# Performance work log

Measured on AMD Instinct MI355X. Metric: run time of the kernel, lower is better.

Reference implementation:

```python
import jax, jax.numpy as jnp
import numpy as np

B, S, D, H, L = 4, 4096, 64, 8, 4
VOCAB, NCLS = 256, 10
MLP = D * H          # mlp_dim = dim * heads = 512
BS = 256             # block size for banded attention
R = 256              # one-sided radius (sliding_window_size = 512)


def sinusoid_pos_emb(s, d):
    pos = np.arange(s)[:, None].astype(np.float32)
    i = np.arange(d // 2)[None, :].astype(np.float32)
    ang = pos / np.power(10000.0, 2.0 * i / d)
    pe = np.zeros((s, d), np.float32)
    pe[:, 0::2] = np.sin(ang)
    pe[:, 1::2] = np.cos(ang)
    return jnp.asarray(pe)


def layernorm(x, s, b):
    m = x.mean(-1, keepdims=True)
    v = ((x - m) ** 2).mean(-1, keepdims=True)
    return (x - m) * jax.lax.rsqrt(v + 1e-6) * s + b


def sliding_window_attn(x, wq, bq, wk, bk, wv, bv, wo, bo):
    Bx, Sx, Dx = x.shape
    Dh = Dx // H
    nb = Sx // BS

    def proj(w, b2):
        return (x @ w + b2).reshape(Bx, Sx, H, Dh).transpose(0, 2, 1, 3)

    q = proj(wq, bq) / jnp.sqrt(jnp.float32(Dh))
    k = proj(wk, bk)
    v = proj(wv, bv)

    def windows(t):  # [B,H,S,Dh] -> [B,H,nb,3*BS,Dh] (prev | self | next blocks)
        tp = jnp.pad(t, ((0, 0), (0, 0), (BS, BS), (0, 0))).reshape(Bx, H, nb + 2, BS, Dh)
        return jnp.concatenate([tp[:, :, :-2], tp[:, :, 1:-1], tp[:, :, 2:]], axis=3)

    kw, vw = windows(k), windows(v)
    qb = q.reshape(Bx, H, nb, BS, Dh)
    scores = jnp.einsum('bhnqd,bhnkd->bhnqk', qb, kw)      # [B,H,nb,BS,3*BS]

    qpos = jnp.arange(BS)[:, None]
    kpos = jnp.arange(3 * BS)[None, :] - BS
    band = jnp.abs(kpos - qpos) <= R                        # [BS,3*BS]
    kglob = jnp.arange(nb)[:, None, None] * BS + kpos[None]  # [nb,1,3*BS]
    valid = (kglob >= 0) & (kglob < Sx)
    mask = band[None] & valid                                # [nb,BS,3*BS]

    scores = jnp.where(mask[None, None], scores, jnp.float32(-1e30))
    probs = jax.nn.softmax(scores, axis=-1)
    out = jnp.einsum('bhnqk,bhnkd->bhnqd', probs, vw)
    out = out.reshape(Bx, H, Sx, Dh).transpose(0, 2, 1, 3).reshape(Bx, Sx, Dx)
    return out @ wo + bo


def setup_inputs() -> dict:
    key = jax.random.key(0)
    ks = jax.random.split(key, 12)
    g = lambda k, shp: jax.random.normal(k, shp, dtype=jnp.float32) * 0.02
    emb = g(ks[0], (VOCAB, D)).at[0].set(0.0)  # padding_idx=0 row is zeros
    return dict(
        x=jax.random.randint(ks[1], (B, S), 0, VOCAB).astype(jnp.int32),
        emb=emb,
        wq=g(ks[2], (L, D, D)), bq=jnp.zeros((L, D)),
        wk=g(ks[3], (L, D, D)), bk=jnp.zeros((L, D)),
        wv=g(ks[4], (L, D, D)), bv=jnp.zeros((L, D)),
        wo=g(ks[5], (L, D, D)), bo=jnp.zeros((L, D)),
        ln1_s=jnp.ones((L, D)), ln1_b=jnp.zeros((L, D)),
        ln2_s=jnp.ones((L, D)), ln2_b=jnp.zeros((L, D)),
        w1=g(ks[6], (L, D, MLP)), b1=jnp.zeros((L, MLP)),
        w2=g(ks[7], (L, MLP, D)), b2=jnp.zeros((L, D)),
        lnf_s=jnp.ones((D,)), lnf_b=jnp.zeros((D,)),
        wcls=g(ks[8], (D, NCLS)), bcls=jnp.zeros((NCLS,)),
    )


def reference(x, emb, wq, bq, wk, bk, wv, bv, wo, bo, ln1_s, ln1_b, ln2_s, ln2_b, w1, b1, w2, b2, lnf_s, lnf_b, wcls, bcls):
    h = emb[x] + sinusoid_pos_emb(S, D)[None]                 # embedding + fixed pos emb
    for l in range(L):
        a = sliding_window_attn(layernorm(h, ln1_s[l], ln1_b[l]),
                                wq[l], bq[l], wk[l], bk[l], wv[l], bv[l], wo[l], bo[l])
        h = h + a
        y = layernorm(h, ln2_s[l], ln2_b[l])
        y = jax.nn.gelu(y @ w1[l] + b1[l]) @ w2[l] + b2[l]
        h = h + y
    h = layernorm(h, lnf_s, lnf_b)
    pooled = h.mean(axis=1)                                   # classifier_pool='MEAN'
    return pooled @ wcls + bcls
```

## Files before the change

### kernel.cpp

```cpp
#include <hip/hip_runtime.h>
#include <hip/hip_bf16.h>

#define DEV __device__ __forceinline__

typedef __attribute__((ext_vector_type(8))) short bf16x8;
typedef __attribute__((ext_vector_type(4))) float f32x4;
typedef __attribute__((ext_vector_type(16))) float f32x16;

DEV short f2bf(float x){ __hip_bfloat16 h = __float2bfloat16(x); return *(short*)&h; }
DEV unsigned pack2bf(float a, float b){
  return (unsigned)(unsigned short)f2bf(a) | ((unsigned)(unsigned short)f2bf(b) << 16);
}
DEV float gelu_fast(float x){
  float z = 0.7978845608028654f*(x + 0.044715f*x*x*x);
  float e = __expf(-2.f*z);
  return x / (1.f + e);
}

#define SB 4096
#define NT 16384
#define DM 64
#define VST 586

__global__ __launch_bounds__(256) void wconv(
    const float* __restrict__ wq, const float* __restrict__ wk,
    const float* __restrict__ wv, const float* __restrict__ wo,
    const float* __restrict__ w1, const float* __restrict__ w2,
    short* __restrict__ wqT, short* __restrict__ wkT,
    short* __restrict__ wvT, short* __restrict__ woT,
    short* __restrict__ w1T, short* __restrict__ w2T)
{
  int t = blockIdx.x, l = blockIdx.y;
  const float* src; short* dst; int K, N, kt, nt;
  if (t < 16) {
    int m = t >> 2, sub = t & 3; kt = sub >> 1; nt = sub & 1; K = 64; N = 64;
    const float* s4[4] = {wq, wk, wv, wo};
    short*       d4[4] = {wqT, wkT, wvT, woT};
    src = s4[m] + l*4096; dst = d4[m] + l*4096;
  } else if (t < 48) {
    kt = (t-16) >> 4; nt = (t-16) & 15; K = 64; N = 512;
    src = w1 + l*32768; dst = w1T + l*32768;
  } else {
    kt = (t-48) >> 1; nt = (t-48) & 1; K = 512; N = 64;
    src = w2 + l*32768; dst = w2T + l*32768;
  }
  __shared__ float lds[32][33];
  int tx = threadIdx.x & 31, ty = threadIdx.x >> 5;
  int k0 = kt*32, n0 = nt*32;
  #pragma unroll
  for (int j=0;j<4;++j) lds[ty+8*j][tx] = src[(size_t)(k0+ty+8*j)*N + n0 + tx];
  __syncthreads();
  #pragma unroll
  for (int j=0;j<4;++j) {
    int nn = ty+8*j;
    dst[(size_t)(n0+nn)*K + k0 + tx] = f2bf(lds[tx][nn]);
  }
}

DEV void make_frags_ln(const float* rowp, float mean, float inv,
    const float* __restrict__ s, const float* __restrict__ b, int kq,
    bf16x8& a0, bf16x8& a1){
  #pragma unroll
  for (int i=0;i<8;++i) a0[i] = f2bf((rowp[kq*8+i]-mean)*inv*s[kq*8+i]+b[kq*8+i]);
  #pragma unroll
  for (int i=0;i<8;++i) a1[i] = f2bf((rowp[32+kq*8+i]-mean)*inv*s[32+kq*8+i]+b[32+kq*8+i]);
}

template<bool EMBED, bool LAST>
__global__ __launch_bounds__(512,2) void layer_kernel(
    const int* __restrict__ x, const float* __restrict__ emb,
    const unsigned short* __restrict__ qin, const unsigned short* __restrict__ kin,
    const unsigned short* __restrict__ vin,
    const short* __restrict__ woT, const float* __restrict__ bo,
    const float* __restrict__ ln2s, const float* __restrict__ ln2b,
    const short* __restrict__ w1T, const float* __restrict__ b1,
    const short* __restrict__ w2T, const float* __restrict__ b2,
    const float* __restrict__ lns, const float* __restrict__ lnb,
    const short* __restrict__ wqT, const short* __restrict__ wkT, const short* __restrict__ wvT,
    const float* __restrict__ bq, const float* __restrict__ bk, const float* __restrict__ bv,
    unsigned short* __restrict__ qo, unsigned short* __restrict__ ko, unsigned short* __restrict__ vo,
    float* __restrict__ h, float* __restrict__ part)
{
  __shared__ uint4 regA4[4608];
  __shared__ uint4 regB4[4688];
  __shared__ float mu[64], iv[64];

  unsigned short* Ks  = (unsigned short*)regA4;
  unsigned short* abL = (unsigned short*)regA4;
  float (*hN)[68]   = (float(*)[68])((char*)regA4 + 9216);
  float (*facc)[68] = (float(*)[68])((char*)regA4 + 26624);
  unsigned short* Vs = (unsigned short*)regB4;
  short (*mid)[520]  = (short(*)[520])regB4;

  const int bid = blockIdx.x;
  const int row_g0 = bid * 64;
  const int tid = threadIdx.x;
  const int w = tid >> 6, lane = tid & 63;
  const int r = lane & 15, kq = lane >> 4;
  const int srow = tid >> 3, sd8 = tid & 7;

  if constexpr (EMBED) {
    int tg = row_g0 + srow;
    int s = tg & (SB-1);
    int tok = x[tg];
    #pragma unroll
    for (int i=0;i<8;++i) {
      int d = sd8*8 + i;
      float fe = (float)(d & ~1) * (1.0f/64.0f);
      float invk = __expf(-9.210340371976184f * fe);
      float ang = (float)s * invk;
      float pe = (d & 1) ? __cosf(ang) : __sinf(ang);
      float val = emb[tok*DM + d] + pe;
      hN[srow][d] = val;
      h[(size_t)tg*DM + d] = val;
    }
  } else {
    const int bbase = row_g0 & ~(SB-1);
    const int kwin0 = row_g0 - 256;

    for (int idx = tid; idx < 4608; idx += 512) {
      int e = idx >> 3, grp = idx & 7;
      int g = kwin0 + e;
      uint4 kv = make_uint4(0,0,0,0), vv = make_uint4(0,0,0,0);
      if ((unsigned)(g - bbase) < (unsigned)SB) {
        kv = *(const uint4*)(kin + (size_t)g*DM + grp*8);
        vv = *(const uint4*)(vin + (size_t)g*DM + grp*8);
      }
      *(uint4*)(Ks + e*64 + ((grp ^ (e & 7)) << 3)) = kv;
      const unsigned short* pv = (const unsigned short*)&vv;
      #pragma unroll
      for (int d = 0; d < 8; ++d) Vs[(grp*8 + d)*VST + e] = pv[d];
    }
    __syncthreads();

    const int qc = lane & 31;
    const int hf = lane >> 5;

    auto attn_job = [&](int qs, f32x16& oacc, float& lacc) {
      const int qglob = row_g0 + qs*32 + qc;
      bf16x8 qfrag = {};
      if (hf == 0) qfrag = *(const bf16x8*)(qin + (size_t)qglob*DM + w*8);
      for (int t = 0; t <= 16; ++t) {
        const int k0l = qs*32 + 32*t;
        const int k0g = kwin0 + k0l;
        if (k0g > bbase + SB-1 || k0g + 31 < bbase) continue;

        bf16x8 kfrag = {};
        if (hf == 0) {
          int e = k0l + qc;
          kfrag = *(const bf16x8*)(Ks + e*64 + ((w ^ (e & 7)) << 3));
        }
        f32x16 s = __builtin_amdgcn_mfma_f32_32x32x16_bf16(kfrag, qfrag, (f32x16){}, 0, 0, 0);

        float pp[16];
        bool needmask = (t == 0) | (t == 16) | (k0g < bbase) | (k0g + 31 > bbase + SB-1);
        if (needmask) {
          #pragma unroll
          for (int rr = 0; rr < 16; ++rr) {
            int klg = k0g + (rr&3) + 8*(rr>>2) + 4*hf;
            bool ok = ((unsigned)(klg - qglob + 256) <= 512u) &&
                      ((unsigned)(klg - bbase) < (unsigned)SB);
            pp[rr] = ok ? __expf(s[rr]) : 0.f;
          }
        } else {
          #pragma unroll
          for (int rr = 0; rr < 16; ++rr) pp[rr] = __expf(s[rr]);
        }
        #pragma unroll
        for (int rr = 0; rr < 16; ++rr) lacc += pp[rr];

        unsigned pk[8];
        #pragma unroll
        for (int j = 0; j < 8; ++j) pk[j] = pack2bf(pp[2*j], pp[2*j+1]);
        unsigned sw[8];
        #pragma unroll
        for (int j = 0; j < 8; ++j) sw[j] = __shfl_xor(pk[j], 32, 64);

        union { unsigned u[4]; bf16x8 v; } pbA;
        pbA.u[0] = hf ? sw[2] : pk[0];
        pbA.u[1] = hf ? sw[3] : pk[1];
        pbA.u[2] = hf ? pk[2] : sw[0];
        pbA.u[3] = hf ? pk[3] : sw[1];
        bf16x8 va1 = {};
        if (qc < 8) va1 = *(const bf16x8*)(Vs + (w*8 + qc)*VST + k0l + 8*hf);
        oacc = __builtin_amdgcn_mfma_f32_32x32x16_bf16(va1, pbA.v, oacc, 0, 0, 0);

        union { unsigned u[4]; bf16x8 v; } pbB;
        pbB.u[0] = hf ? sw[6] : pk[4];
        pbB.u[1] = hf ? sw[7] : pk[5];
        pbB.u[2] = hf ? pk[6] : sw[4];
        pbB.u[3] = hf ? pk[7] : sw[5];
        bf16x8 va2 = {};
        if (qc < 8) va2 = *(const bf16x8*)(Vs + (w*8 + qc)*VST + k0l + 16 + 8*hf);
        oacc = __builtin_amdgcn_mfma_f32_32x32x16_bf16(va2, pbB.v, oacc, 0, 0, 0);
      }
    };

    f32x16 oacc0 = {}; float la0 = 0.f;
    f32x16 oacc1 = {}; float la1 = 0.f;
    attn_job(0, oacc0, la0);
    attn_job(1, oacc1, la1);
    float rcp0 = 1.f / (la0 + __shfl_xor(la0, 32, 64));
    float rcp1 = 1.f / (la1 + __shfl_xor(la1, 32, 64));
    __syncthreads();

    {
      unsigned short ov[4];
      #pragma unroll
      for (int j = 0; j < 4; ++j) ov[j] = (unsigned short)f2bf(oacc0[j] * rcp0);
      *(uint2*)(abL + (qc)*72 + w*8 + 4*hf) = *(uint2*)ov;
      #pragma unroll
      for (int j = 0; j < 4; ++j) ov[j] = (unsigned short)f2bf(oacc1[j] * rcp1);
      *(uint2*)(abL + (32 + qc)*72 + w*8 + 4*hf) = *(uint2*)ov;
    }
    __syncthreads();

    {
      const int rh = w >> 2, ct = w & 3;
      const int col = ct*16 + r;
      const short* wp = woT + (size_t)col*64 + kq*8;
      bf16x8 wb0 = *(const bf16x8*)(wp);
      bf16x8 wb1 = *(const bf16x8*)(wp + 32);
      #pragma unroll
      for (int rf=0; rf<2; ++rf) {
        const short* abp = (const short*)(abL + (rh*32 + rf*16 + r)*72 + kq*8);
        bf16x8 a0 = *(const bf16x8*)abp;
        bf16x8 a1 = *(const bf16x8*)(abp + 32);
        f32x4 acc = (f32x4){0.f,0.f,0.f,0.f};
        acc = __builtin_amdgcn_mfma_f32_16x16x32_bf16(a0, wb0, acc, 0, 0, 0);
        acc = __builtin_amdgcn_mfma_f32_16x16x32_bf16(a1, wb1, acc, 0, 0, 0);
        #pragma unroll
        for (int j=0;j<4;++j) {
          int rl = rh*32 + rf*16 + kq*4 + j;
          hN[rl][col] = acc[j] + bo[col] + h[(size_t)(row_g0+rl)*DM + col];
        }
      }
    }
  }
  __syncthreads();

  {
    const float* p = &hN[srow][sd8*8];
    float v[8];
    float sum = 0.f;
    #pragma unroll
    for (int i=0;i<8;++i){ v[i] = p[i]; sum += v[i]; }
    sum += __shfl_xor(sum, 1, 64); sum += __shfl_xor(sum, 2, 64); sum += __shfl_xor(sum, 4, 64);
    float mean = sum * (1.f/64.f);
    float sq = 0.f;
    #pragma unroll
    for (int i=0;i<8;++i){ float d = v[i]-mean; sq += d*d; }
    sq += __shfl_xor(sq, 1, 64); sq += __shfl_xor(sq, 2, 64); sq += __shfl_xor(sq, 4, 64);
    if (sd8 == 0) { mu[srow] = mean; iv[srow] = rsqrtf(sq*(1.f/64.f) + 1e-6f); }
  }
  __syncthreads();

  if constexpr (!EMBED) {
    {
      bf16x8 a[4][2];
      #pragma unroll
      for (int rf=0; rf<4; ++rf)
        make_frags_ln(&hN[rf*16 + r][0], mu[rf*16 + r], iv[rf*16 + r], ln2s, ln2b, kq, a[rf][0], a[rf][1]);
      const int gc0 = w*64;
      bf16x8 wb[4][2];
      #pragma unroll
      for (int ct=0; ct<4; ++ct) {
        const short* wp = w1T + (size_t)(gc0 + ct*16 + r)*64 + kq*8;
        wb[ct][0] = *(const bf16x8*)(wp);
        wb[ct][1] = *(const bf16x8*)(wp + 32);
      }
      f32x4 acc1[4][4];
      #pragma unroll
      for (int ct=0;ct<4;++ct)
        #pragma unroll
        for (int rf=0;rf<4;++rf) acc1[ct][rf] = (f32x4){0.f,0.f,0.f,0.f};
      #pragma unroll
      for (int ct=0; ct<4; ++ct)
        #pragma unroll
        for (int rf=0; rf<4; ++rf) {
          acc1[ct][rf] = __builtin_amdgcn_mfma_f32_16x16x32_bf16(a[rf][0], wb[ct][0], acc1[ct][rf], 0, 0, 0);
          acc1[ct][rf] = __builtin_amdgcn_mfma_f32_16x16x32_bf16(a[rf][1], wb[ct][1], acc1[ct][rf], 0, 0, 0);
        }
      __syncthreads();
      #pragma unroll
      for (int ct=0; ct<4; ++ct) {
        int gcol = gc0 + ct*16 + r;
        float bb = b1[gcol];
        #pragma unroll
        for (int rf=0; rf<4; ++rf)
          #pragma unroll
          for (int j=0; j<4; ++j)
            mid[rf*16 + kq*4 + j][gcol] = f2bf(gelu_fast(acc1[ct][rf][j] + bb));
      }
    }
    __syncthreads();

    {
      const int kh = w >> 2, ct2 = w & 3;
      const int col2 = ct2*16 + r;
      bf16x8 wf[8];
      #pragma unroll
      for (int ks=0; ks<8; ++ks)
        wf[ks] = *(const bf16x8*)(w2T + (size_t)col2*512 + kh*256 + ks*32 + kq*8);
      f32x4 acc2[4];
      #pragma unroll
      for (int rf=0;rf<4;++rf) acc2[rf] = (f32x4){0.f,0.f,0.f,0.f};
      #pragma unroll
      for (int ks=0; ks<8; ++ks)
        #pragma unroll
        for (int rf=0; rf<4; ++rf) {
          bf16x8 af = *(const bf16x8*)(&mid[rf*16 + r][kh*256 + ks*32 + kq*8]);
          acc2[rf] = __builtin_amdgcn_mfma_f32_16x16x32_bf16(af, wf[ks], acc2[rf], 0, 0, 0);
        }
      if (kh == 0) {
        #pragma unroll
        for (int rf=0; rf<4; ++rf)
          #pragma unroll
          for (int j=0;j<4;++j)
            facc[rf*16 + kq*4 + j][col2] = acc2[rf][j];
      }
      __syncthreads();
      if (kh == 1) {
        float bb = b2[col2];
        #pragma unroll
        for (int rf=0; rf<4; ++rf)
          #pragma unroll
          for (int j=0;j<4;++j) {
            int rl = rf*16 + kq*4 + j;
            float val = acc2[rf][j] + facc[rl][col2] + bb + hN[rl][col2];
            hN[rl][col2] = val;
            h[(size_t)(row_g0+rl)*DM + col2] = val;
          }
      }
    }
    __syncthreads();

    {
      const float* p = &hN[srow][sd8*8];
      float v[8];
      float sum = 0.f;
      #pragma unroll
      for (int i=0;i<8;++i){ v[i] = p[i]; sum += v[i]; }
      sum += __shfl_xor(sum, 1, 64); sum += __shfl_xor(sum, 2, 64); sum += __shfl_xor(sum, 4, 64);
      float mean = sum * (1.f/64.f);
      float sq = 0.f;
      #pragma unroll
      for (int i=0;i<8;++i){ float d = v[i]-mean; sq += d*d; }
      sq += __shfl_xor(sq, 1, 64); sq += __shfl_xor(sq, 2, 64); sq += __shfl_xor(sq, 4, 64);
      if (sd8 == 0) { mu[srow] = mean; iv[srow] = rsqrtf(sq*(1.f/64.f) + 1e-6f); }
    }
    __syncthreads();
  }

  if constexpr (!LAST) {
    const float qscale = 0.35355339059327373f;
    bf16x8 a[4][2];
    #pragma unroll
    for (int rf=0; rf<4; ++rf)
      make_frags_ln(&hN[rf*16 + r][0], mu[rf*16 + r], iv[rf*16 + r], lns, lnb, kq, a[rf][0], a[rf][1]);
    #pragma unroll
    for (int rep=0; rep<2; ++rep) {
      int jj = w + rep*8;
      if (jj < 12) {
        int m = jj >> 2, ct = jj & 3;
        const short* WT = m==0 ? wqT : (m==1 ? wkT : wvT);
        int col = ct*16 + r;
        const short* wp = WT + (size_t)col*64 + kq*8;
        bf16x8 wb0 = *(const bf16x8*)(wp);
        bf16x8 wb1 = *(const bf16x8*)(wp + 32);
        float bias = (m==0 ? bq : (m==1 ? bk : bv))[col];
        float scale = (m==0) ? qscale : 1.f;
        unsigned short* OPT = m==0 ? qo : (m==1 ? ko : vo);
        #pragma unroll
        for (int rf=0; rf<4; ++rf) {
          f32x4 acc = (f32x4){0.f,0.f,0.f,0.f};
          acc = __builtin_amdgcn_mfma_f32_16x16x32_bf16(a[rf][0], wb0, acc, 0, 0, 0);
          acc = __builtin_amdgcn_mfma_f32_16x16x32_bf16(a[rf][1], wb1, acc, 0, 0, 0);
          #pragma unroll
          for (int j=0;j<4;++j) {
            size_t oi = (size_t)(row_g0 + rf*16 + kq*4 + j)*DM + col;
            OPT[oi] = (unsigned short)f2bf((acc[j] + bias)*scale);
          }
        }
      }
    }
  } else {
    float mean = mu[srow], inv = iv[srow];
    #pragma unroll
    for (int i=0;i<8;++i) {
      int d = sd8*8 + i;
      hN[srow][d] = (hN[srow][d]-mean)*inv*lns[d] + lnb[d];
    }
    __syncthreads();
    if (tid < 64) {
      float s = 0.f;
      #pragma unroll 4
      for (int rr=0; rr<64; ++rr) s += hN[rr][tid];
      part[bid*64 + tid] = s;
    }
  }
}

__global__ __launch_bounds__(256) void pool_finalize(const float* __restrict__ part,
    const float* __restrict__ wcls, const float* __restrict__ bcls, float* __restrict__ out)
{
  int tid = threadIdx.x;
  int b = tid >> 6, d = tid & 63;
  float sum = 0.f;
  #pragma unroll 8
  for (int i = 0; i < 64; ++i) sum += part[(b*64 + i)*64 + d];
  __shared__ float pooled[4][64];
  pooled[b][d] = sum * (1.f/4096.f);
  __syncthreads();
  if (tid < 40) {
    int bb = tid / 10, c = tid % 10;
    float acc = bcls[c];
    #pragma unroll
    for (int dd = 0; dd < 64; ++dd) acc = fmaf(pooled[bb][dd], wcls[dd*10 + c], acc);
    out[tid] = acc;
  }
}

extern "C" void kernel_launch(void* const* d_in, const int* in_sizes, int n_in,
                              void* d_out, int out_size, void* d_ws, size_t ws_size,
                              hipStream_t stream)
{
  const int*   x    = (const int*)d_in[0];
  const float* emb  = (const float*)d_in[1];
  const float* wq   = (const float*)d_in[2];
  const float* bq   = (const float*)d_in[3];
  const float* wk   = (const float*)d_in[4];
  const float* bk   = (const float*)d_in[5];
  const float* wv   = (const float*)d_in[6];
  const float* bv   = (const float*)d_in[7];
  const float* wo   = (const float*)d_in[8];
  const float* bo   = (const float*)d_in[9];
  const float* ln1s = (const float*)d_in[10];
  const float* ln1b = (const float*)d_in[11];
  const float* ln2s = (const float*)d_in[12];
  const float* ln2b = (const float*)d_in[13];
  const float* w1   = (const float*)d_in[14];
  const float* b1   = (const float*)d_in[15];
  const float* w2   = (const float*)d_in[16];
  const float* b2   = (const float*)d_in[17];
  const float* lnfs = (const float*)d_in[18];
  const float* lnfb = (const float*)d_in[19];
  const float* wcls = (const float*)d_in[20];
  const float* bcls = (const float*)d_in[21];
  float* out = (float*)d_out;

  char* wsb = (char*)d_ws;
  const size_t MB = 1u << 20;
  float* h  = (float*)(wsb);
  unsigned short* qA = (unsigned short*)(wsb + 4*MB);
  unsigned short* kA = (unsigned short*)(wsb + 6*MB);
  unsigned short* vA = (unsigned short*)(wsb + 8*MB);
  unsigned short* qB = (unsigned short*)(wsb + 10*MB);
  unsigned short* kB = (unsigned short*)(wsb + 12*MB);
  unsigned short* vB = (unsigned short*)(wsb + 14*MB);
  short* wqT = (short*)(wsb + 16*MB);
  short* wkT = (short*)(wsb + 16*MB + 32*1024);
  short* wvT = (short*)(wsb + 16*MB + 64*1024);
  short* woT = (short*)(wsb + 16*MB + 96*1024);
  short* w1T = (short*)(wsb + 16*MB + 128*1024);
  short* w2T = (short*)(wsb + 16*MB + 384*1024);
  float* part = (float*)(wsb + 17*MB);

  wconv<<<dim3(80,4),256,0,stream>>>(wq,wk,wv,wo,w1,w2, wqT,wkT,wvT,woT,w1T,w2T);

  layer_kernel<true,false><<<256,512,0,stream>>>(
      x, emb, nullptr, nullptr, nullptr,
      nullptr, nullptr, nullptr, nullptr,
      nullptr, nullptr, nullptr, nullptr,
      ln1s, ln1b,
      wqT, wkT, wvT, bq, bk, bv,
      qA, kA, vA, h, nullptr);

  for (int l = 0; l < 4; ++l) {
    unsigned short* qi = (l & 1) ? qB : qA;
    unsigned short* ki = (l & 1) ? kB : kA;
    unsigned short* vi = (l & 1) ? vB : vA;
    unsigned short* qu = (l & 1) ? qA : qB;
    unsigned short* ku = (l & 1) ? kA : kB;
    unsigned short* vu = (l & 1) ? vA : vB;
    if (l < 3) {
      layer_kernel<false,false><<<256,512,0,stream>>>(
          nullptr, nullptr, qi, ki, vi,
          woT+4096*l, bo+64*l, ln2s+64*l, ln2b+64*l,
          w1T+32768*l, b1+512*l, w2T+32768*l, b2+64*l,
          ln1s+64*(l+1), ln1b+64*(l+1),
          wqT+4096*(l+1), wkT+4096*(l+1), wvT+4096*(l+1),
          bq+64*(l+1), bk+64*(l+1), bv+64*(l+1),
          qu, ku, vu, h, nullptr);
    } else {
      layer_kernel<false,true><<<256,512,0,stream>>>(
          nullptr, nullptr, qi, ki, vi,
          woT+4096*l, bo+64*l, ln2s+64*l, ln2b+64*l,
          w1T+32768*l, b1+512*l, w2T+32768*l, b2+64*l,
          lnfs, lnfb,
          nullptr, nullptr, nullptr, nullptr, nullptr, nullptr,
          nullptr, nullptr, nullptr, h, part);
    }
  }
  pool_finalize<<<1,256,0,stream>>>(part, wcls, bcls, out);
}
```

Measured before the change: 184.4 us.

## Double workgroup size to 1024 threads and split per-wave work in half

Result: no change. 182.5 us (-1.0%).

```diff
diff --git a/kernel.cpp b/kernel.cpp
--- a/kernel.cpp
+++ b/kernel.cpp
@@ -67,7 +67,7 @@
 }
 
 template<bool EMBED, bool LAST>
-__global__ __launch_bounds__(512,2) void layer_kernel(
+__global__ __launch_bounds__(1024,1) void layer_kernel(
     const int* __restrict__ x, const float* __restrict__ emb,
     const unsigned short* __restrict__ qin, const unsigned short* __restrict__ kin,
     const unsigned short* __restrict__ vin,
@@ -97,15 +97,15 @@
   const int tid = threadIdx.x;
   const int w = tid >> 6, lane = tid & 63;
   const int r = lane & 15, kq = lane >> 4;
-  const int srow = tid >> 3, sd8 = tid & 7;
+  const int srow = tid >> 4, sd4 = tid & 15;
 
   if constexpr (EMBED) {
     int tg = row_g0 + srow;
     int s = tg & (SB-1);
     int tok = x[tg];
     #pragma unroll
-    for (int i=0;i<8;++i) {
-      int d = sd8*8 + i;
+    for (int i=0;i<4;++i) {
+      int d = sd4*4 + i;
       float fe = (float)(d & ~1) * (1.0f/64.0f);
       float invk = __expf(-9.210340371976184f * fe);
       float ang = (float)s * invk;
@@ -118,7 +118,7 @@
     const int bbase = row_g0 & ~(SB-1);
     const int kwin0 = row_g0 - 256;
 
-    for (int idx = tid; idx < 4608; idx += 512) {
+    for (int idx = tid; idx < 4608; idx += 1024) {
       int e = idx >> 3, grp = idx & 7;
       int g = kwin0 + e;
       uint4 kv = make_uint4(0,0,0,0), vv = make_uint4(0,0,0,0);
@@ -135,11 +135,14 @@
 
     const int qc = lane & 31;
     const int hf = lane >> 5;
-
-    auto attn_job = [&](int qs, f32x16& oacc, float& lacc) {
+    const int hh = w >> 1, qs = w & 1;
+
+    f32x16 oacc = {};
+    float lacc = 0.f;
+    {
       const int qglob = row_g0 + qs*32 + qc;
       bf16x8 qfrag = {};
-      if (hf == 0) qfrag = *(const bf16x8*)(qin + (size_t)qglob*DM + w*8);
+      if (hf == 0) qfrag = *(const bf16x8*)(qin + (size_t)qglob*DM + hh*8);
       for (int t = 0; t <= 16; ++t) {
         const int k0l = qs*32 + 32*t;
         const int k0g = kwin0 + k0l;
@@ -148,7 +151,7 @@
         bf16x8 kfrag = {};
         if (hf == 0) {
           int e = k0l + qc;
-          kfrag = *(const bf16x8*)(Ks + e*64 + ((w ^ (e & 7)) << 3));
+          kfrag = *(const bf16x8*)(Ks + e*64 + ((hh ^ (e & 7)) << 3));
         }
         f32x16 s = __builtin_amdgcn_mfma_f32_32x32x16_bf16(kfrag, qfrag, (f32x16){}, 0, 0, 0);
 
@@ -182,7 +185,7 @@
         pbA.u[2] = hf ? pk[2] : sw[0];
         pbA.u[3] = hf ? pk[3] : sw[1];
         bf16x8 va1 = {};
-        if (qc < 8) va1 = *(const bf16x8*)(Vs + (w*8 + qc)*VST + k0l + 8*hf);
+        if (qc < 8) va1 = *(const bf16x8*)(Vs + (hh*8 + qc)*VST + k0l + 8*hf);
         oacc = __builtin_amdgcn_mfma_f32_32x32x16_bf16(va1, pbA.v, oacc, 0, 0, 0);
 
         union { unsigned u[4]; bf16x8 v; } pbB;
@@ -191,27 +194,18 @@
         pbB.u[2] = hf ? pk[6] : sw[4];
         pbB.u[3] = hf ? pk[7] : sw[5];
         bf16x8 va2 = {};
-        if (qc < 8) va2 = *(const bf16x8*)(Vs + (w*8 + qc)*VST + k0l + 16 + 8*hf);
+        if (qc < 8) va2 = *(const bf16x8*)(Vs + (hh*8 + qc)*VST + k0l + 16 + 8*hf);
         oacc = __builtin_amdgcn_mfma_f32_32x32x16_bf16(va2, pbB.v, oacc, 0, 0, 0);
       }
-    };
-
-    f32x16 oacc0 = {}; float la0 = 0.f;
-    f32x16 oacc1 = {}; float la1 = 0.f;
-    attn_job(0, oacc0, la0);
-    attn_job(1, oacc1, la1);
-    float rcp0 = 1.f / (la0 + __shfl_xor(la0, 32, 64));
-    float rcp1 = 1.f / (la1 + __shfl_xor(la1, 32, 64));
+    }
+    float rcp = 1.f / (lacc + __shfl_xor(lacc, 32, 64));
     __syncthreads();
 
     {
       unsigned short ov[4];
       #pragma unroll
-      for (int j = 0; j < 4; ++j) ov[j] = (unsigned short)f2bf(oacc0[j] * rcp0);
-      *(uint2*)(abL + (qc)*72 + w*8 + 4*hf) = *(uint2*)ov;
-      #pragma unroll
-      for (int j = 0; j < 4; ++j) ov[j] = (unsigned short)f2bf(oacc1[j] * rcp1);
-      *(uint2*)(abL + (32 + qc)*72 + w*8 + 4*hf) = *(uint2*)ov;
+      for (int j = 0; j < 4; ++j) ov[j] = (unsigned short)f2bf(oacc[j] * rcp);
+      *(uint2*)(abL + (qs*32 + qc)*72 + hh*8 + 4*hf) = *(uint2*)ov;
     }
     __syncthreads();
 
@@ -221,37 +215,33 @@
       const short* wp = woT + (size_t)col*64 + kq*8;
       bf16x8 wb0 = *(const bf16x8*)(wp);
       bf16x8 wb1 = *(const bf16x8*)(wp + 32);
-      #pragma unroll
-      for (int rf=0; rf<2; ++rf) {
-        const short* abp = (const short*)(abL + (rh*32 + rf*16 + r)*72 + kq*8);
-        bf16x8 a0 = *(const bf16x8*)abp;
-        bf16x8 a1 = *(const bf16x8*)(abp + 32);
-        f32x4 acc = (f32x4){0.f,0.f,0.f,0.f};
-        acc = __builtin_amdgcn_mfma_f32_16x16x32_bf16(a0, wb0, acc, 0, 0, 0);
-        acc = __builtin_amdgcn_mfma_f32_16x16x32_bf16(a1, wb1, acc, 0, 0, 0);
-        #pragma unroll
-        for (int j=0;j<4;++j) {
-          int rl = rh*32 + rf*16 + kq*4 + j;
-          hN[rl][col] = acc[j] + bo[col] + h[(size_t)(row_g0+rl)*DM + col];
-        }
+      const short* abp = (const short*)(abL + (rh*16 + r)*72 + kq*8);
+      bf16x8 a0 = *(const bf16x8*)abp;
+      bf16x8 a1 = *(const bf16x8*)(abp + 32);
+      f32x4 acc = (f32x4){0.f,0.f,0.f,0.f};
+      acc = __builtin_amdgcn_mfma_f32_16x16x32_bf16(a0, wb0, acc, 0, 0, 0);
+      acc = __builtin_amdgcn_mfma_f32_16x16x32_bf16(a1, wb1, acc, 0, 0, 0);
+      #pragma unroll
+      for (int j=0;j<4;++j) {
+        int rl = rh*16 + kq*4 + j;
+        hN[rl][col] = acc[j] + bo[col] + h[(size_t)(row_g0+rl)*DM + col];
       }
     }
   }
   __syncthreads();
 
   {
-    const float* p = &hN[srow][sd8*8];
-    float v[8];
-    float sum = 0.f;
-    #pragma unroll
-    for (int i=0;i<8;++i){ v[i] = p[i]; sum += v[i]; }
-    sum += __shfl_xor(sum, 1, 64); sum += __shfl_xor(sum, 2, 64); sum += __shfl_xor(sum, 4, 64);
+    const float* p = &hN[srow][sd4*4];
+    float v0=p[0], v1=p[1], v2=p[2], v3=p[3];
+    float sum = v0+v1+v2+v3;
+    sum += __shfl_xor(sum, 1, 64); sum += __shfl_xor(sum, 2, 64);
+    sum += __shfl_xor(sum, 4, 64); sum += __shfl_xor(sum, 8, 64);
     float mean = sum * (1.f/64.f);
-    float sq = 0.f;
-    #pragma unroll
-    for (int i=0;i<8;++i){ float d = v[i]-mean; sq += d*d; }
-    sq += __shfl_xor(sq, 1, 64); sq += __shfl_xor(sq, 2, 64); sq += __shfl_xor(sq, 4, 64);
-    if (sd8 == 0) { mu[srow] = mean; iv[srow] = rsqrtf(sq*(1.f/64.f) + 1e-6f); }
+    float d0=v0-mean, d1=v1-mean, d2=v2-mean, d3=v3-mean;
+    float sq = d0*d0+d1*d1+d2*d2+d3*d3;
+    sq += __shfl_xor(sq, 1, 64); sq += __shfl_xor(sq, 2, 64);
+    sq += __shfl_xor(sq, 4, 64); sq += __shfl_xor(sq, 8, 64);
+    if (sd4 == 0) { mu[srow] = mean; iv[srow] = rsqrtf(sq*(1.f/64.f) + 1e-6f); }
   }
   __syncthreads();
 
@@ -261,21 +251,21 @@
       #pragma unroll
       for (int rf=0; rf<4; ++rf)
         make_frags_ln(&hN[rf*16 + r][0], mu[rf*16 + r], iv[rf*16 + r], ln2s, ln2b, kq, a[rf][0], a[rf][1]);
-      const int gc0 = w*64;
-      bf16x8 wb[4][2];
-      #pragma unroll
-      for (int ct=0; ct<4; ++ct) {
+      const int gc0 = w*32;
+      bf16x8 wb[2][2];
+      #pragma unroll
+      for (int ct=0; ct<2; ++ct) {
         const short* wp = w1T + (size_t)(gc0 + ct*16 + r)*64 + kq*8;
         wb[ct][0] = *(const bf16x8*)(wp);
         wb[ct][1] = *(const bf16x8*)(wp + 32);
       }
-      f32x4 acc1[4][4];
-      #pragma unroll
-      for (int ct=0;ct<4;++ct)
+      f32x4 acc1[2][4];
+      #pragma unroll
+      for (int ct=0;ct<2;++ct)
         #pragma unroll
         for (int rf=0;rf<4;++rf) acc1[ct][rf] = (f32x4){0.f,0.f,0.f,0.f};
       #pragma unroll
-      for (int ct=0; ct<4; ++ct)
+      for (int ct=0; ct<2; ++ct)
         #pragma unroll
         for (int rf=0; rf<4; ++rf) {
           acc1[ct][rf] = __builtin_amdgcn_mfma_f32_16x16x32_bf16(a[rf][0], wb[ct][0], acc1[ct][rf], 0, 0, 0);
@@ -283,7 +273,7 @@
         }
       __syncthreads();
       #pragma unroll
-      for (int ct=0; ct<4; ++ct) {
+      for (int ct=0; ct<2; ++ct) {
         int gcol = gc0 + ct*16 + r;
         float bb = b1[gcol];
         #pragma unroll
@@ -296,37 +286,38 @@
     __syncthreads();
 
     {
-      const int kh = w >> 2, ct2 = w & 3;
+      const int kh = w >> 3, rh2 = (w >> 2) & 1, ct2 = w & 3;
       const int col2 = ct2*16 + r;
+      const int rbase = rh2*32;
       bf16x8 wf[8];
       #pragma unroll
       for (int ks=0; ks<8; ++ks)
         wf[ks] = *(const bf16x8*)(w2T + (size_t)col2*512 + kh*256 + ks*32 + kq*8);
-      f32x4 acc2[4];
-      #pragma unroll
-      for (int rf=0;rf<4;++rf) acc2[rf] = (f32x4){0.f,0.f,0.f,0.f};
+      f32x4 acc2[2];
+      #pragma unroll
+      for (int rf=0;rf<2;++rf) acc2[rf] = (f32x4){0.f,0.f,0.f,0.f};
       #pragma unroll
       for (int ks=0; ks<8; ++ks)
         #pragma unroll
-        for (int rf=0; rf<4; ++rf) {
-          bf16x8 af = *(const bf16x8*)(&mid[rf*16 + r][kh*256 + ks*32 + kq*8]);
+        for (int rf=0; rf<2; ++rf) {
+          bf16x8 af = *(const bf16x8*)(&mid[rbase + rf*16 + r][kh*256 + ks*32 + kq*8]);
           acc2[rf] = __builtin_amdgcn_mfma_f32_16x16x32_bf16(af, wf[ks], acc2[rf], 0, 0, 0);
         }
       if (kh == 0) {
         #pragma unroll
-        for (int rf=0; rf<4; ++rf)
+        for (int rf=0; rf<2; ++rf)
           #pragma unroll
           for (int j=0;j<4;++j)
-            facc[rf*16 + kq*4 + j][col2] = acc2[rf][j];
+            facc[rbase + rf*16 + kq*4 + j][col2] = acc2[rf][j];
       }
       __syncthreads();
       if (kh == 1) {
         float bb = b2[col2];
         #pragma unroll
-        for (int rf=0; rf<4; ++rf)
+        for (int rf=0; rf<2; ++rf)
           #pragma unroll
           for (int j=0;j<4;++j) {
-            int rl = rf*16 + kq*4 + j;
+            int rl = rbase + rf*16 + kq*4 + j;
             float val = acc2[rf][j] + facc[rl][col2] + bb + hN[rl][col2];
             hN[rl][col2] = val;
             h[(size_t)(row_g0+rl)*DM + col2] = val;
@@ -336,59 +327,54 @@
     __syncthreads();
 
     {
-      const float* p = &hN[srow][sd8*8];
-      float v[8];
-      float sum = 0.f;
-      #pragma unroll
-      for (int i=0;i<8;++i){ v[i] = p[i]; sum += v[i]; }
-      sum += __shfl_xor(sum, 1, 64); sum += __shfl_xor(sum, 2, 64); sum += __shfl_xor(sum, 4, 64);
+      const float* p = &hN[srow][sd4*4];
+      float v0=p[0], v1=p[1], v2=p[2], v3=p[3];
+      float sum = v0+v1+v2+v3;
+      sum += __shfl_xor(sum, 1, 64); sum += __shfl_xor(sum, 2, 64);
+      sum += __shfl_xor(sum, 4, 64); sum += __shfl_xor(sum, 8, 64);
       float mean = sum * (1.f/64.f);
-      float sq = 0.f;
-      #pragma unroll
-      for (int i=0;i<8;++i){ float d = v[i]-mean; sq += d*d; }
-      sq += __shfl_xor(sq, 1, 64); sq += __shfl_xor(sq, 2, 64); sq += __shfl_xor(sq, 4, 64);
-      if (sd8 == 0) { mu[srow] = mean; iv[srow] = rsqrtf(sq*(1.f/64.f) + 1e-6f); }
+      float d0=v0-mean, d1=v1-mean, d2=v2-mean, d3=v3-mean;
+      float sq = d0*d0+d1*d1+d2*d2+d3*d3;
+      sq += __shfl_xor(sq, 1, 64); sq += __shfl_xor(sq, 2, 64);
+      sq += __shfl_xor(sq, 4, 64); sq += __shfl_xor(sq, 8, 64);
+      if (sd4 == 0) { mu[srow] = mean; iv[srow] = rsqrtf(sq*(1.f/64.f) + 1e-6f); }
     }
     __syncthreads();
   }
 
   if constexpr (!LAST) {
     const float qscale = 0.35355339059327373f;
-    bf16x8 a[4][2];
-    #pragma unroll
-    for (int rf=0; rf<4; ++rf)
-      make_frags_ln(&hN[rf*16 + r][0], mu[rf*16 + r], iv[rf*16 + r], lns, lnb, kq, a[rf][0], a[rf][1]);
-    #pragma unroll
-    for (int rep=0; rep<2; ++rep) {
-      int jj = w + rep*8;
-      if (jj < 12) {
-        int m = jj >> 2, ct = jj & 3;
-        const short* WT = m==0 ? wqT : (m==1 ? wkT : wvT);
-        int col = ct*16 + r;
-        const short* wp = WT + (size_t)col*64 + kq*8;
-        bf16x8 wb0 = *(const bf16x8*)(wp);
-        bf16x8 wb1 = *(const bf16x8*)(wp + 32);
-        float bias = (m==0 ? bq : (m==1 ? bk : bv))[col];
-        float scale = (m==0) ? qscale : 1.f;
-        unsigned short* OPT = m==0 ? qo : (m==1 ? ko : vo);
-        #pragma unroll
-        for (int rf=0; rf<4; ++rf) {
-          f32x4 acc = (f32x4){0.f,0.f,0.f,0.f};
-          acc = __builtin_amdgcn_mfma_f32_16x16x32_bf16(a[rf][0], wb0, acc, 0, 0, 0);
-          acc = __builtin_amdgcn_mfma_f32_16x16x32_bf16(a[rf][1], wb1, acc, 0, 0, 0);
-          #pragma unroll
-          for (int j=0;j<4;++j) {
-            size_t oi = (size_t)(row_g0 + rf*16 + kq*4 + j)*DM + col;
-            OPT[oi] = (unsigned short)f2bf((acc[j] + bias)*scale);
-          }
+    if (w < 12) {
+      bf16x8 a[4][2];
+      #pragma unroll
+      for (int rf=0; rf<4; ++rf)
+        make_frags_ln(&hN[rf*16 + r][0], mu[rf*16 + r], iv[rf*16 + r], lns, lnb, kq, a[rf][0], a[rf][1]);
+      int m = w >> 2, ct = w & 3;
+      const short* WT = m==0 ? wqT : (m==1 ? wkT : wvT);
+      int col = ct*16 + r;
+      const short* wp = WT + (size_t)col*64 + kq*8;
+      bf16x8 wb0 = *(const bf16x8*)(wp);
+      bf16x8 wb1 = *(const bf16x8*)(wp + 32);
+      float bias = (m==0 ? bq : (m==1 ? bk : bv))[col];
+      float scale = (m==0) ? qscale : 1.f;
+      unsigned short* OPT = m==0 ? qo : (m==1 ? ko : vo);
+      #pragma unroll
+      for (int rf=0; rf<4; ++rf) {
+        f32x4 acc = (f32x4){0.f,0.f,0.f,0.f};
+        acc = __builtin_amdgcn_mfma_f32_16x16x32_bf16(a[rf][0], wb0, acc, 0, 0, 0);
+        acc = __builtin_amdgcn_mfma_f32_16x16x32_bf16(a[rf][1], wb1, acc, 0, 0, 0);
+        #pragma unroll
+        for (int j=0;j<4;++j) {
+          size_t oi = (size_t)(row_g0 + rf*16 + kq*4 + j)*DM + col;
+          OPT[oi] = (unsigned short)f2bf((acc[j] + bias)*scale);
         }
       }
     }
   } else {
     float mean = mu[srow], inv = iv[srow];
     #pragma unroll
-    for (int i=0;i<8;++i) {
-      int d = sd8*8 + i;
+    for (int i=0;i<4;++i) {
+      int d = sd4*4 + i;
       hN[srow][d] = (hN[srow][d]-mean)*inv*lns[d] + lnb[d];
     }
     __syncthreads();
@@ -468,7 +454,7 @@
 
   wconv<<<dim3(80,4),256,0,stream>>>(wq,wk,wv,wo,w1,w2, wqT,wkT,wvT,woT,w1T,w2T);
 
-  layer_kernel<true,false><<<256,512,0,stream>>>(
+  layer_kernel<true,false><<<256,1024,0,stream>>>(
       x, emb, nullptr, nullptr, nullptr,
       nullptr, nullptr, nullptr, nullptr,
       nullptr, nullptr, nullptr, nullptr,
@@ -484,7 +470,7 @@
     unsigned short* ku = (l & 1) ? kA : kB;
     unsigned short* vu = (l & 1) ? vA : vB;
     if (l < 3) {
-      layer_kernel<false,false><<<256,512,0,stream>>>(
+      layer_kernel<false,false><<<256,1024,0,stream>>>(
           nullptr, nullptr, qi, ki, vi,
           woT+4096*l, bo+64*l, ln2s+64*l, ln2b+64*l,
           w1T+32768*l, b1+512*l, w2T+32768*l, b2+64*l,
@@ -493,7 +479,7 @@
           bq+64*(l+1), bk+64*(l+1), bv+64*(l+1),
           qu, ku, vu, h, nullptr);
     } else {
-      layer_kernel<false,true><<<256,512,0,stream>>>(
+      layer_kernel<false,true><<<256,1024,0,stream>>>(
           nullptr, nullptr, qi, ki, vi,
           woT+4096*l, bo+64*l, ln2s+64*l, ln2b+64*l,
           w1T+32768*l, b1+512*l, w2T+32768*l, b2+64*l,
```
